# Kernel tuning notes

Hardware: AMD Instinct MI355X
Metric: run time of the kernel (lower is better)

Reference implementation:

```python
import jax, jax.numpy as jnp
import numpy as np

B, S, E, M, N, H = 16, 4096, 1024, 64, 32, 8
MIN_NODES = 3

def _ln(x, w, b, eps=1e-5):
    mu = jnp.mean(x, axis=-1, keepdims=True)
    var = jnp.mean((x - mu) ** 2, axis=-1, keepdims=True)
    return (x - mu) / jnp.sqrt(var + eps) * w + b

def setup_inputs():
    ks = jax.random.split(jax.random.key(0), 16)
    f32 = jnp.float32
    r = lambda i, shape, s: jax.random.normal(ks[i], shape, dtype=f32) * s
    return {
        "x": jax.random.normal(ks[0], (B, S, E), dtype=f32),
        "task_query": jax.random.normal(ks[1], (1, 1, E), dtype=f32),
        "wq": r(2, (E, E), 0.02), "bq": jnp.zeros((E,), f32),
        "wk": r(3, (E, E), 0.02), "bk": jnp.zeros((E,), f32),
        "wv": r(4, (E, E), 0.02), "bv": jnp.zeros((E,), f32),
        "wo": r(5, (E, E), 0.02), "bo": jnp.zeros((E,), f32),
        "mp_w": r(6, (M, E), 0.02), "mp_b": jnp.zeros((M,), f32),
        "ln_w": jnp.ones((M,), f32), "ln_b": jnp.zeros((M,), f32),
        "ng_w1": r(7, (2 * M, M), 0.05), "ng_b1": jnp.zeros((2 * M,), f32),
        "ng_w2": r(8, (N * M, 2 * M), 0.05), "ng_b2": jnp.zeros((N * M,), f32),
        "imp_w": r(9, (1, M), 0.1), "imp_b": jnp.zeros((1,), f32),
        "ep_w": r(10, (1, M, M), 0.05), "ep_b": jnp.zeros((1,), f32),
        "cp_w1": r(11, (M // 2, M), 0.1), "cp_b1": jnp.zeros((M // 2,), f32),
        "cp_w2": r(12, (1, M // 2), 0.1), "cp_b2": jnp.zeros((1,), f32),
        "np_w": r(13, (E, M), 0.05), "np_b": jnp.zeros((E,), f32),
    }

def reference(x, task_query, wq, bq, wk, bk, wv, bv, wo, bo, mp_w, mp_b,
              ln_w, ln_b, ng_w1, ng_b1, ng_w2, ng_b2, imp_w, imp_b,
              ep_w, ep_b, cp_w1, cp_b1, cp_w2, cp_b2, np_w, np_b):
    Bx, Sx, Ex = x.shape
    D = Ex // H
    # multi-head attention: single learned task query attends over x (q_len=1)
    q = jnp.broadcast_to(task_query, (Bx, 1, Ex)) @ wq.T + bq
    k = x @ wk.T + bk
    v = x @ wv.T + bv
    qh = q.reshape(Bx, 1, H, D).transpose(0, 2, 1, 3)
    kh = k.reshape(Bx, Sx, H, D).transpose(0, 2, 1, 3)
    vh = v.reshape(Bx, Sx, H, D).transpose(0, 2, 1, 3)
    attn = jax.nn.softmax(jnp.einsum('bhqd,bhkd->bhqk', qh, kh) / jnp.sqrt(jnp.float32(D)), axis=-1)
    ctx = jnp.einsum('bhqk,bhkd->bhqd', attn, vh).transpose(0, 2, 1, 3).reshape(Bx, 1, Ex)
    task_repr = (ctx @ wo.T + bo)[:, 0, :]  # (B, E)
    # manifold projection + node generation
    tm = _ln(task_repr @ mp_w.T + mp_b, ln_w, ln_b)  # (B, M)
    h = jax.nn.gelu(tm @ ng_w1.T + ng_b1, approximate=False)
    nm = (h @ ng_w2.T + ng_b2).reshape(Bx, N, M)
    nm = _ln(nm, ln_w, ln_b)  # (B, N, M)
    # deterministic node selection via top-k importance
    importance = nm @ imp_w[0] + imp_b[0]  # (B, N)
    k_nodes = max(MIN_NODES, min(N, Sx // 2 + 1))
    _, top_idx = jax.lax.top_k(importance, k_nodes)
    node_mask = jnp.zeros((Bx, N), dtype=bool).at[jnp.arange(Bx)[:, None], top_idx].set(True)
    # pairwise bilinear edge scoring as ONE batched contraction (replaces NxN python loop)
    edge_logits = jnp.einsum('bim,mn,bjn->bij', nm, ep_w[0], nm) + ep_b[0]
    dag_mask = jnp.triu(jnp.ones((N, N), x.dtype), k=1)
    pair_mask = (node_mask[:, :, None] & node_mask[:, None, :]).astype(x.dtype)
    adj = jax.nn.sigmoid(edge_logits) * dag_mask * pair_mask
    adj_matrix = (adj > 0.3).astype(x.dtype)
    # complexity / surface area
    c = jax.nn.gelu(nm @ cp_w1.T + cp_b1, approximate=False)
    c = (c @ cp_w2.T + cp_b2)[..., 0]
    complexities = jax.nn.softplus(c) * node_mask.astype(x.dtype)
    surface_area = complexities.sum(-1)
    node_embeddings = nm @ np_w.T + np_b  # (B, N, E)
    return node_embeddings, adj_matrix, surface_area, complexities, node_mask
```

## Files before the change

### kernel.cpp

```cpp
#include <hip/hip_runtime.h>
#include <hip/hip_bf16.h>


#define DEVFN __device__ __forceinline__

constexpr float SCALE = 0.08838834764831845f;

constexpr size_t OFF_QVEC  = 0;
constexpr size_t OFF_QKT   = 1024;
constexpr size_t OFF_QB    = 9216;
constexpr size_t OFF_LPART = 9224;
constexpr size_t OFF_CTX   = 13320;
constexpr size_t OFF_TREP  = 29704;
constexpr size_t OFF_TM    = 46088;
constexpr size_t OFF_NMG   = 47112;
constexpr size_t OFF_PART  = 79880;

constexpr size_t OUT_EMB  = 0;
constexpr size_t OUT_ADJ  = 524288;
constexpr size_t OUT_SURF = 540672;
constexpr size_t OUT_CPLX = 540688;
constexpr size_t OUT_MASK = 541200;

DEVFN float gelu_exact(float x) {
  return 0.5f * x * (1.0f + erff(x * 0.70710678118654752f));
}
DEVFN float softplus_f(float x) {
  return fmaxf(x, 0.0f) + log1pf(expf(-fabsf(x)));
}
DEVFN float dot4(float4 a, float4 b) {
  return a.x * b.x + a.y * b.y + a.z * b.z + a.w * b.w;
}

__global__ void k_qvec(const float* __restrict__ tq, const float* __restrict__ wq,
                       const float* __restrict__ bq, float* __restrict__ qvec) {
  int wid = threadIdx.x >> 6, lane = threadIdx.x & 63;
  int i = blockIdx.x * 4 + wid;
  const float* wrow = wq + (size_t)i * 1024;
  float acc = 0.f;
#pragma unroll
  for (int k = 0; k < 4; ++k) {
    int e = lane * 4 + k * 256;
    acc += dot4(*(const float4*)(tq + e), *(const float4*)(wrow + e));
  }
#pragma unroll
  for (int off = 32; off; off >>= 1) acc += __shfl_xor(acc, off);
  if (lane == 0) qvec[i] = acc + bq[i];
}

__global__ void k_qk(const float* __restrict__ qvec, const float* __restrict__ wk,
                     const float* __restrict__ bk, float* __restrict__ qkT,
                     float* __restrict__ qb) {
  __shared__ float qh[128];
  int h = blockIdx.x >> 2, e0 = (blockIdx.x & 3) * 256;
  int t = threadIdx.x;
  if (t < 128) qh[t] = qvec[h * 128 + t];
  __syncthreads();
  int e = e0 + t;
  float acc = 0.f;
#pragma unroll 32
  for (int d = 0; d < 128; ++d)
    acc += qh[d] * wk[(size_t)(h * 128 + d) * 1024 + e];
  qkT[h * 1024 + e] = acc * SCALE;
  if (t == 0 && e0 == 0) {
    float s = 0.f;
    for (int d = 0; d < 128; ++d) s += qh[d] * bk[h * 128 + d];
    qb[h] = s * SCALE;
  }
}

__global__ __launch_bounds__(256, 2) void k_fused(
    const float* __restrict__ x, const float* __restrict__ qkT,
    const float* __restrict__ qb, float* __restrict__ partial,
    float* __restrict__ lpart) {
  __shared__ __align__(16) float lds[8 * 1024];
  __shared__ float s_ll[8];
  int t = threadIdx.x, wid = t >> 6, lane = t & 63;
  int rh = wid >> 1, hg = wid & 1;

  float4 qr[4][4];
#pragma unroll
  for (int hh = 0; hh < 4; ++hh)
#pragma unroll
    for (int k = 0; k < 4; ++k)
      qr[hh][k] = *(const float4*)(qkT + (hg * 4 + hh) * 1024 + k * 256 + lane * 4);
  float qbr[4];
#pragma unroll
  for (int hh = 0; hh < 4; ++hh) qbr[hh] = qb[hg * 4 + hh];

  float4 acc[4][4];
#pragma unroll
  for (int hh = 0; hh < 4; ++hh)
#pragma unroll
    for (int k = 0; k < 4; ++k) acc[hh][k] = make_float4(0.f, 0.f, 0.f, 0.f);
  float lsum[4] = {0.f, 0.f, 0.f, 0.f};

  int row0 = blockIdx.x * 128 + rh * 64;
  const float* xr = x + ((size_t)row0 << 10) + lane * 4;
  float4 A0 = *(const float4*)(xr + 0);
  float4 A1 = *(const float4*)(xr + 256);
  float4 A2 = *(const float4*)(xr + 512);
  float4 A3 = *(const float4*)(xr + 768);
  float4 B0 = *(const float4*)(xr + 1024);
  float4 B1 = *(const float4*)(xr + 1280);
  float4 B2 = *(const float4*)(xr + 1536);
  float4 B3 = *(const float4*)(xr + 1792);

  for (int r = 0; r < 64; ++r) {
    float4 c0 = A0, c1 = A1, c2 = A2, c3 = A3;
    A0 = B0; A1 = B1; A2 = B2; A3 = B3;
    if (r < 62) {
      const float* nx = xr + ((size_t)(r + 2) << 10);
      B0 = *(const float4*)(nx + 0);
      B1 = *(const float4*)(nx + 256);
      B2 = *(const float4*)(nx + 512);
      B3 = *(const float4*)(nx + 768);
    }
    float s[4];
#pragma unroll
    for (int hh = 0; hh < 4; ++hh)
      s[hh] = dot4(c0, qr[hh][0]) + dot4(c1, qr[hh][1]) +
              dot4(c2, qr[hh][2]) + dot4(c3, qr[hh][3]);
#pragma unroll
    for (int off = 1; off <= 32; off <<= 1)
#pragma unroll
      for (int hh = 0; hh < 4; ++hh) s[hh] += __shfl_xor(s[hh], off);
    float w[4];
#pragma unroll
    for (int hh = 0; hh < 4; ++hh) {
      w[hh] = expf(s[hh] + qbr[hh]);
      lsum[hh] += w[hh];
    }
#pragma unroll
    for (int hh = 0; hh < 4; ++hh) {
      acc[hh][0].x += w[hh] * c0.x; acc[hh][0].y += w[hh] * c0.y;
      acc[hh][0].z += w[hh] * c0.z; acc[hh][0].w += w[hh] * c0.w;
      acc[hh][1].x += w[hh] * c1.x; acc[hh][1].y += w[hh] * c1.y;
      acc[hh][1].z += w[hh] * c1.z; acc[hh][1].w += w[hh] * c1.w;
      acc[hh][2].x += w[hh] * c2.x; acc[hh][2].y += w[hh] * c2.y;
      acc[hh][2].z += w[hh] * c2.z; acc[hh][2].w += w[hh] * c2.w;
      acc[hh][3].x += w[hh] * c3.x; acc[hh][3].y += w[hh] * c3.y;
      acc[hh][3].z += w[hh] * c3.z; acc[hh][3].w += w[hh] * c3.w;
    }
  }
  if (rh == 1) {
#pragma unroll
    for (int hh = 0; hh < 4; ++hh)
#pragma unroll
      for (int k = 0; k < 4; ++k)
        *(float4*)(lds + (hg * 4 + hh) * 1024 + k * 256 + lane * 4) = acc[hh][k];
    if (lane == 0)
#pragma unroll
      for (int hh = 0; hh < 4; ++hh) s_ll[hg * 4 + hh] = lsum[hh];
  }
  __syncthreads();
  if (rh == 0) {
    size_t base = (((size_t)blockIdx.x * 8 + hg * 4) << 10) + lane * 4;
#pragma unroll
    for (int hh = 0; hh < 4; ++hh)
#pragma unroll
      for (int k = 0; k < 4; ++k) {
        const float4 o = *(const float4*)(lds + (hg * 4 + hh) * 1024 + k * 256 + lane * 4);
        float4 v = acc[hh][k];
        v.x += o.x; v.y += o.y; v.z += o.z; v.w += o.w;
        *(float4*)(partial + base + ((size_t)hh << 10) + k * 256) = v;
      }
    if (lane == 0)
#pragma unroll
      for (int hh = 0; hh < 4; ++hh)
        lpart[blockIdx.x * 8 + hg * 4 + hh] = lsum[hh] + s_ll[hg * 4 + hh];
  }
}

__global__ __launch_bounds__(256) void k_combctx(
    const float* __restrict__ partial, const float* __restrict__ lpart,
    const float* __restrict__ wv, const float* __restrict__ bv,
    float* __restrict__ ctx) {
  __shared__ __align__(16) float s_xa[1024];
  __shared__ float s_linv;
  int bh = blockIdx.x, b = bh >> 3, h = bh & 7, t = threadIdx.x;
  float4 s4 = make_float4(0.f, 0.f, 0.f, 0.f);
#pragma unroll 8
  for (int c = 0; c < 32; ++c) {
    float4 v = *(const float4*)(partial +
        (((size_t)(b * 32 + c) * 8 + h) << 10) + t * 4);
    s4.x += v.x; s4.y += v.y; s4.z += v.z; s4.w += v.w;
  }
  *(float4*)(s_xa + t * 4) = s4;
  if (t == 0) {
    float s = 0.f;
#pragma unroll
    for (int c = 0; c < 32; ++c) s += lpart[(b * 32 + c) * 8 + h];
    s_linv = 1.0f / s;
  }
  __syncthreads();
  int wid = t >> 6, lane = t & 63;
  float linv = s_linv;
  for (int it = 0; it < 32; ++it) {
    int j = h * 128 + wid * 32 + it;
    const float* wr = wv + (size_t)j * 1024 + lane * 4;
    const float* xr = s_xa + lane * 4;
    float acc = 0.f;
#pragma unroll
    for (int k = 0; k < 4; ++k)
      acc += dot4(*(const float4*)(xr + k * 256), *(const float4*)(wr + k * 256));
#pragma unroll
    for (int off = 32; off; off >>= 1) acc += __shfl_xor(acc, off);
    if (lane == 0) ctx[b * 1024 + j] = acc * linv + bv[j];
  }
}

__global__ void k_trep(const float* __restrict__ ctx, const float* __restrict__ wo,
                       const float* __restrict__ bo, float* __restrict__ trep) {
  int wid = threadIdx.x >> 6, lane = threadIdx.x & 63;
#pragma unroll
  for (int it = 0; it < 4; ++it) {
    int gw = blockIdx.x * 16 + wid * 4 + it;
    int b = gw >> 10, i = gw & 1023;
    const float* xr = ctx + (size_t)b * 1024;
    const float* wr = wo + (size_t)i * 1024;
    float acc = 0.f;
#pragma unroll
    for (int k = 0; k < 4; ++k) {
      int e = lane * 4 + k * 256;
      acc += dot4(*(const float4*)(xr + e), *(const float4*)(wr + e));
    }
#pragma unroll
    for (int off = 32; off; off >>= 1) acc += __shfl_xor(acc, off);
    if (lane == 0) trep[b * 1024 + i] = acc + bo[i];
  }
}

__global__ void k_tm(const float* __restrict__ trep, const float* __restrict__ mp_w,
                     const float* __restrict__ mp_b, float* __restrict__ tmg) {
  int b = blockIdx.x >> 2, mc = blockIdx.x & 3;
  int wid = threadIdx.x >> 6, lane = threadIdx.x & 63;
  const float* xr = trep + (size_t)b * 1024 + lane * 4;
#pragma unroll
  for (int it = 0; it < 4; ++it) {
    int m = mc * 16 + wid * 4 + it;
    const float* wr = mp_w + (size_t)m * 1024 + lane * 4;
    float acc = 0.f;
#pragma unroll
    for (int k = 0; k < 4; ++k)
      acc += dot4(*(const float4*)(xr + k * 256), *(const float4*)(wr + k * 256));
#pragma unroll
    for (int off = 32; off; off >>= 1) acc += __shfl_xor(acc, off);
    if (lane == 0) tmg[b * 64 + m] = acc + mp_b[m];
  }
}

__global__ __launch_bounds__(256) void k_nm(
    const float* __restrict__ tmg, const float* __restrict__ ln_w,
    const float* __restrict__ ln_b, const float* __restrict__ ng_w1,
    const float* __restrict__ ng_b1, const float* __restrict__ ng_w2,
    const float* __restrict__ ng_b2, float* __restrict__ nmg) {
  __shared__ float s_tm[64];
  __shared__ float s_h2[128];
  __shared__ float s_np[128];
  int b = blockIdx.x >> 4, np = blockIdx.x & 15;
  int t = threadIdx.x, wid = t >> 6, lane = t & 63;
  if (wid == 0) {
    float v = tmg[b * 64 + lane];
    float sm = v;
#pragma unroll
    for (int off = 32; off; off >>= 1) sm += __shfl_xor(sm, off);
    float mu = sm * (1.f / 64.f);
    float d = v - mu;
    float vv = d * d;
#pragma unroll
    for (int off = 32; off; off >>= 1) vv += __shfl_xor(vv, off);
    float rstd = 1.f / sqrtf(vv * (1.f / 64.f) + 1e-5f);
    s_tm[lane] = d * rstd * ln_w[lane] + ln_b[lane];
  }
  __syncthreads();
  if (t < 128) {
    float acc = ng_b1[t];
    const float* wr = ng_w1 + (size_t)t * 64;
#pragma unroll 16
    for (int m = 0; m < 64; ++m) acc += s_tm[m] * wr[m];
    s_h2[t] = gelu_exact(acc);
  }
  __syncthreads();
  if (t < 128) {
    int o = np * 128 + t;
    float acc = ng_b2[o];
    const float* wr = ng_w2 + (size_t)o * 128;
#pragma unroll 8
    for (int r = 0; r < 128; ++r) acc += s_h2[r] * wr[r];
    s_np[t] = acc;
  }
  __syncthreads();
  if (wid < 2) {
    float v = s_np[wid * 64 + lane];
    float sm = v;
#pragma unroll
    for (int off = 32; off; off >>= 1) sm += __shfl_xor(sm, off);
    float mu = sm * (1.f / 64.f);
    float d = v - mu;
    float vv = d * d;
#pragma unroll
    for (int off = 32; off; off >>= 1) vv += __shfl_xor(vv, off);
    float rstd = 1.f / sqrtf(vv * (1.f / 64.f) + 1e-5f);
    nmg[b * 2048 + (np * 2 + wid) * 64 + lane] = d * rstd * ln_w[lane] + ln_b[lane];
  }
}

__global__ __launch_bounds__(256) void k_headsemb(
    const float* __restrict__ nmg, const float* __restrict__ ep_w,
    const float* __restrict__ ep_b, const float* __restrict__ cp_w1,
    const float* __restrict__ cp_b1, const float* __restrict__ cp_w2,
    const float* __restrict__ cp_b2, const float* __restrict__ np_w,
    const float* __restrict__ np_b, float* __restrict__ out) {
  __shared__ __align__(16) float s_nm[2048];
  __shared__ float s_t[2048];
  __shared__ float s_c1[1024];
  __shared__ float s_cx[32];
  int t = threadIdx.x, wid = t >> 6, lane = t & 63;
  if (blockIdx.x < 16) {
    int b = blockIdx.x;
    for (int i = t; i < 512; i += 256)
      ((float4*)s_nm)[i] = ((const float4*)(nmg + (size_t)b * 2048))[i];
    __syncthreads();
    for (int o = t; o < 1024; o += 256) {
      int i = o >> 5, r = o & 31;
      float acc = cp_b1[r];
      const float* wr = cp_w1 + (size_t)r * 64;
#pragma unroll 8
      for (int m = 0; m < 64; ++m) acc += s_nm[i * 64 + m] * wr[m];
      s_c1[o] = gelu_exact(acc);
    }
    __syncthreads();
    if (t < 32) {
      float acc = cp_b2[0];
#pragma unroll 8
      for (int r = 0; r < 32; ++r) acc += s_c1[t * 32 + r] * cp_w2[r];
      float sp = softplus_f(acc);
      s_cx[t] = sp;
      out[OUT_CPLX + b * 32 + t] = sp;
      out[OUT_MASK + b * 32 + t] = 1.0f;
    }
    __syncthreads();
    if (wid == 0) {
      float v = (lane < 32) ? s_cx[lane] : 0.f;
#pragma unroll
      for (int off = 32; off; off >>= 1) v += __shfl_xor(v, off);
      if (lane == 0) out[OUT_SURF + b] = v;
    }
    for (int o = t; o < 2048; o += 256) {
      int i = o >> 6, n = o & 63;
      float acc = 0.f;
#pragma unroll 8
      for (int m = 0; m < 64; ++m) acc += s_nm[i * 64 + m] * ep_w[m * 64 + n];
      s_t[o] = acc;
    }
    __syncthreads();
    for (int o = t; o < 1024; o += 256) {
      int i = o >> 5, j = o & 31;
      float acc = ep_b[0];
#pragma unroll 8
      for (int n = 0; n < 64; ++n) acc += s_t[i * 64 + n] * s_nm[j * 64 + n];
      float sg = 1.f / (1.f + expf(-acc));
      float val = (j > i && sg > 0.3f) ? 1.f : 0.f;
      out[OUT_ADJ + (size_t)b * 1024 + i * 32 + j] = val;
    }
  } else {
    int idx = blockIdx.x - 16;
    int b = idx >> 2, e0 = (idx & 3) * 256;
    *(float4*)(s_nm + t * 4) = *(const float4*)(nmg + b * 2048 + t * 4);
    *(float4*)(s_nm + 1024 + t * 4) =
        *(const float4*)(nmg + b * 2048 + 1024 + t * 4);
    __syncthreads();
    int e = e0 + t;
    float4 w[16];
    const float* wr = np_w + (size_t)e * 64;
#pragma unroll
    for (int k = 0; k < 16; ++k) w[k] = *(const float4*)(wr + k * 4);
    float bias = np_b[e];
    for (int i = 0; i < 32; ++i) {
      float acc = bias;
#pragma unroll
      for (int k = 0; k < 16; ++k)
        acc += dot4(w[k], *(const float4*)(s_nm + i * 64 + k * 4));
      out[OUT_EMB + (size_t)(b * 32 + i) * 1024 + e] = acc;
    }
  }
}

extern "C" void kernel_launch(void* const* d_in, const int* in_sizes, int n_in,
                              void* d_out, int out_size, void* d_ws, size_t ws_size,
                              hipStream_t stream) {
  (void)in_sizes; (void)n_in; (void)out_size; (void)ws_size;
  const float* x    = (const float*)d_in[0];
  const float* tq   = (const float*)d_in[1];
  const float* wq   = (const float*)d_in[2];
  const float* bq   = (const float*)d_in[3];
  const float* wk   = (const float*)d_in[4];
  const float* bk   = (const float*)d_in[5];
  const float* wv   = (const float*)d_in[6];
  const float* bv   = (const float*)d_in[7];
  const float* wo   = (const float*)d_in[8];
  const float* bo   = (const float*)d_in[9];
  const float* mp_w = (const float*)d_in[10];
  const float* mp_b = (const float*)d_in[11];
  const float* ln_w = (const float*)d_in[12];
  const float* ln_b = (const float*)d_in[13];
  const float* ng_w1 = (const float*)d_in[14];
  const float* ng_b1 = (const float*)d_in[15];
  const float* ng_w2 = (const float*)d_in[16];
  const float* ng_b2 = (const float*)d_in[17];
  const float* ep_w  = (const float*)d_in[20];
  const float* ep_b  = (const float*)d_in[21];
  const float* cp_w1 = (const float*)d_in[22];
  const float* cp_b1 = (const float*)d_in[23];
  const float* cp_w2 = (const float*)d_in[24];
  const float* cp_b2 = (const float*)d_in[25];
  const float* np_w  = (const float*)d_in[26];
  const float* np_b  = (const float*)d_in[27];

  float* out = (float*)d_out;
  float* ws = (float*)d_ws;
  float* qvec    = ws + OFF_QVEC;
  float* qkT     = ws + OFF_QKT;
  float* qb      = ws + OFF_QB;
  float* lpart   = ws + OFF_LPART;
  float* ctx     = ws + OFF_CTX;
  float* trep    = ws + OFF_TREP;
  float* tmg     = ws + OFF_TM;
  float* nmg     = ws + OFF_NMG;
  float* partial = ws + OFF_PART;

  k_qvec<<<256, 256, 0, stream>>>(tq, wq, bq, qvec);
  k_qk<<<32, 256, 0, stream>>>(qvec, wk, bk, qkT, qb);
  k_fused<<<512, 256, 0, stream>>>(x, qkT, qb, partial, lpart);
  k_combctx<<<128, 256, 0, stream>>>(partial, lpart, wv, bv, ctx);
  k_trep<<<1024, 256, 0, stream>>>(ctx, wo, bo, trep);
  k_tm<<<64, 256, 0, stream>>>(trep, mp_w, mp_b, tmg);
  k_nm<<<256, 256, 0, stream>>>(tmg, ln_w, ln_b, ng_w1, ng_b1, ng_w2, ng_b2, nmg);
  k_headsemb<<<80, 256, 0, stream>>>(nmg, ep_w, ep_b, cp_w1, cp_b1, cp_w2,
                                     cp_b2, np_w, np_b, out);
}
```

Before: 178.3 us.

## Fuse tail kernels into one persistent kernel with software grid barriers

Merges the five post-attention kernels (ctx combine, output projection, mp projection, node generation, heads/embeddings) into a single 128-block kernel that separates stages with an atomic-counter grid barrier. The aim is to remove four kernel launch gaps on a tail made of small, latency-bound GEMVs. The wo projection now runs on 128 blocks instead of 1024, and the ng_w2 GEMV is restructured with half-wave float4 dot products. The risks are reduced parallelism for the wo GEMV, barrier spin overhead, and reliance on all 128 blocks being co-resident. An extra memset is added to reset the barrier counters.

```diff
diff --git a/kernel.cpp b/kernel.cpp
--- a/kernel.cpp
+++ b/kernel.cpp
@@ -15,6 +15,7 @@
 constexpr size_t OFF_TM    = 46088;
 constexpr size_t OFF_NMG   = 47112;
 constexpr size_t OFF_PART  = 79880;
+constexpr size_t OFF_BAR   = 4274184;
 
 constexpr size_t OUT_EMB  = 0;
 constexpr size_t OUT_ADJ  = 524288;
@@ -22,6 +23,8 @@
 constexpr size_t OUT_CPLX = 540688;
 constexpr size_t OUT_MASK = 541200;
 
+constexpr int TAIL_BLOCKS = 128;
+
 DEVFN float gelu_exact(float x) {
   return 0.5f * x * (1.0f + erff(x * 0.70710678118654752f));
 }
@@ -30,6 +33,29 @@
 }
 DEVFN float dot4(float4 a, float4 b) {
   return a.x * b.x + a.y * b.y + a.z * b.z + a.w * b.w;
+}
+
+DEVFN void grid_sync(int* counter, unsigned int* gen) {
+  __threadfence();
+  __syncthreads();
+  if (threadIdx.x == 0) {
+    unsigned int g = __hip_atomic_load(gen, __ATOMIC_ACQUIRE,
+                                       __HIP_MEMORY_SCOPE_AGENT);
+    int arrived = __hip_atomic_fetch_add(counter, 1, __ATOMIC_ACQ_REL,
+                                         __HIP_MEMORY_SCOPE_AGENT) + 1;
+    if (arrived == TAIL_BLOCKS) {
+      __hip_atomic_store(counter, 0, __ATOMIC_RELAXED,
+                         __HIP_MEMORY_SCOPE_AGENT);
+      __hip_atomic_fetch_add(gen, 1u, __ATOMIC_ACQ_REL,
+                             __HIP_MEMORY_SCOPE_AGENT);
+    } else {
+      while (__hip_atomic_load(gen, __ATOMIC_ACQUIRE,
+                               __HIP_MEMORY_SCOPE_AGENT) == g)
+        __builtin_amdgcn_s_sleep(2);
+    }
+  }
+  __syncthreads();
+  __threadfence();
 }
 
 __global__ void k_qvec(const float* __restrict__ tq, const float* __restrict__ wq,
@@ -140,7 +166,7 @@
       acc[hh][2].x += w[hh] * c2.x; acc[hh][2].y += w[hh] * c2.y;
       acc[hh][2].z += w[hh] * c2.z; acc[hh][2].w += w[hh] * c2.w;
       acc[hh][3].x += w[hh] * c3.x; acc[hh][3].y += w[hh] * c3.y;
-      acc[hh][3].z += w[hh] * c3.z; acc[hh][3].w += w[hh] * c3.w;
+      acc[hh][3].w += w[hh] * c3.w; acc[hh][3].z += w[hh] * c3.z;
     }
   }
   if (rh == 1) {
@@ -172,153 +198,161 @@
   }
 }
 
-__global__ __launch_bounds__(256) void k_combctx(
+__global__ __launch_bounds__(256) void k_tailp(
     const float* __restrict__ partial, const float* __restrict__ lpart,
     const float* __restrict__ wv, const float* __restrict__ bv,
-    float* __restrict__ ctx) {
-  __shared__ __align__(16) float s_xa[1024];
-  __shared__ float s_linv;
-  int bh = blockIdx.x, b = bh >> 3, h = bh & 7, t = threadIdx.x;
-  float4 s4 = make_float4(0.f, 0.f, 0.f, 0.f);
+    const float* __restrict__ wo, const float* __restrict__ bo,
+    const float* __restrict__ mp_w, const float* __restrict__ mp_b,
+    const float* __restrict__ ln_w, const float* __restrict__ ln_b,
+    const float* __restrict__ ng_w1, const float* __restrict__ ng_b1,
+    const float* __restrict__ ng_w2, const float* __restrict__ ng_b2,
+    const float* __restrict__ ep_w, const float* __restrict__ ep_b,
+    const float* __restrict__ cp_w1, const float* __restrict__ cp_b1,
+    const float* __restrict__ cp_w2, const float* __restrict__ cp_b2,
+    const float* __restrict__ np_w, const float* __restrict__ np_b,
+    float* __restrict__ ctx, float* __restrict__ trep,
+    float* __restrict__ tmg, float* __restrict__ nmg,
+    int* __restrict__ bar_counter, unsigned int* __restrict__ bar_gen,
+    float* __restrict__ out) {
+  __shared__ __align__(16) float smem[5184];
+  __shared__ float s_misc;
+  int blk = blockIdx.x, t = threadIdx.x, wid = t >> 6, lane = t & 63;
+
+  {
+    int b = blk >> 3, h = blk & 7;
+    float4 s4 = make_float4(0.f, 0.f, 0.f, 0.f);
 #pragma unroll 8
-  for (int c = 0; c < 32; ++c) {
-    float4 v = *(const float4*)(partial +
-        (((size_t)(b * 32 + c) * 8 + h) << 10) + t * 4);
-    s4.x += v.x; s4.y += v.y; s4.z += v.z; s4.w += v.w;
-  }
-  *(float4*)(s_xa + t * 4) = s4;
-  if (t == 0) {
-    float s = 0.f;
-#pragma unroll
-    for (int c = 0; c < 32; ++c) s += lpart[(b * 32 + c) * 8 + h];
-    s_linv = 1.0f / s;
-  }
-  __syncthreads();
-  int wid = t >> 6, lane = t & 63;
-  float linv = s_linv;
-  for (int it = 0; it < 32; ++it) {
-    int j = h * 128 + wid * 32 + it;
-    const float* wr = wv + (size_t)j * 1024 + lane * 4;
-    const float* xr = s_xa + lane * 4;
-    float acc = 0.f;
-#pragma unroll
-    for (int k = 0; k < 4; ++k)
-      acc += dot4(*(const float4*)(xr + k * 256), *(const float4*)(wr + k * 256));
-#pragma unroll
-    for (int off = 32; off; off >>= 1) acc += __shfl_xor(acc, off);
-    if (lane == 0) ctx[b * 1024 + j] = acc * linv + bv[j];
-  }
-}
-
-__global__ void k_trep(const float* __restrict__ ctx, const float* __restrict__ wo,
-                       const float* __restrict__ bo, float* __restrict__ trep) {
-  int wid = threadIdx.x >> 6, lane = threadIdx.x & 63;
-#pragma unroll
-  for (int it = 0; it < 4; ++it) {
-    int gw = blockIdx.x * 16 + wid * 4 + it;
-    int b = gw >> 10, i = gw & 1023;
-    const float* xr = ctx + (size_t)b * 1024;
-    const float* wr = wo + (size_t)i * 1024;
-    float acc = 0.f;
-#pragma unroll
-    for (int k = 0; k < 4; ++k) {
-      int e = lane * 4 + k * 256;
-      acc += dot4(*(const float4*)(xr + e), *(const float4*)(wr + e));
-    }
-#pragma unroll
-    for (int off = 32; off; off >>= 1) acc += __shfl_xor(acc, off);
-    if (lane == 0) trep[b * 1024 + i] = acc + bo[i];
-  }
-}
-
-__global__ void k_tm(const float* __restrict__ trep, const float* __restrict__ mp_w,
-                     const float* __restrict__ mp_b, float* __restrict__ tmg) {
-  int b = blockIdx.x >> 2, mc = blockIdx.x & 3;
-  int wid = threadIdx.x >> 6, lane = threadIdx.x & 63;
-  const float* xr = trep + (size_t)b * 1024 + lane * 4;
-#pragma unroll
-  for (int it = 0; it < 4; ++it) {
-    int m = mc * 16 + wid * 4 + it;
-    const float* wr = mp_w + (size_t)m * 1024 + lane * 4;
-    float acc = 0.f;
-#pragma unroll
-    for (int k = 0; k < 4; ++k)
-      acc += dot4(*(const float4*)(xr + k * 256), *(const float4*)(wr + k * 256));
-#pragma unroll
-    for (int off = 32; off; off >>= 1) acc += __shfl_xor(acc, off);
-    if (lane == 0) tmg[b * 64 + m] = acc + mp_b[m];
-  }
-}
-
-__global__ __launch_bounds__(256) void k_nm(
-    const float* __restrict__ tmg, const float* __restrict__ ln_w,
-    const float* __restrict__ ln_b, const float* __restrict__ ng_w1,
-    const float* __restrict__ ng_b1, const float* __restrict__ ng_w2,
-    const float* __restrict__ ng_b2, float* __restrict__ nmg) {
-  __shared__ float s_tm[64];
-  __shared__ float s_h2[128];
-  __shared__ float s_np[128];
-  int b = blockIdx.x >> 4, np = blockIdx.x & 15;
-  int t = threadIdx.x, wid = t >> 6, lane = t & 63;
-  if (wid == 0) {
-    float v = tmg[b * 64 + lane];
-    float sm = v;
-#pragma unroll
-    for (int off = 32; off; off >>= 1) sm += __shfl_xor(sm, off);
-    float mu = sm * (1.f / 64.f);
-    float d = v - mu;
-    float vv = d * d;
-#pragma unroll
-    for (int off = 32; off; off >>= 1) vv += __shfl_xor(vv, off);
-    float rstd = 1.f / sqrtf(vv * (1.f / 64.f) + 1e-5f);
-    s_tm[lane] = d * rstd * ln_w[lane] + ln_b[lane];
-  }
-  __syncthreads();
-  if (t < 128) {
-    float acc = ng_b1[t];
-    const float* wr = ng_w1 + (size_t)t * 64;
+    for (int c = 0; c < 32; ++c) {
+      float4 v = *(const float4*)(partial +
+          (((size_t)(b * 32 + c) * 8 + h) << 10) + t * 4);
+      s4.x += v.x; s4.y += v.y; s4.z += v.z; s4.w += v.w;
+    }
+    *(float4*)(smem + t * 4) = s4;
+    if (t == 0) {
+      float s = 0.f;
+#pragma unroll
+      for (int c = 0; c < 32; ++c) s += lpart[(b * 32 + c) * 8 + h];
+      s_misc = 1.0f / s;
+    }
+    __syncthreads();
+    float linv = s_misc;
+    for (int it = 0; it < 32; ++it) {
+      int j = h * 128 + wid * 32 + it;
+      const float* wr = wv + (size_t)j * 1024 + lane * 4;
+      const float* xr = smem + lane * 4;
+      float acc = 0.f;
+#pragma unroll
+      for (int k = 0; k < 4; ++k)
+        acc += dot4(*(const float4*)(xr + k * 256), *(const float4*)(wr + k * 256));
+#pragma unroll
+      for (int off = 32; off; off >>= 1) acc += __shfl_xor(acc, off);
+      if (lane == 0) ctx[b * 1024 + j] = acc * linv + bv[j];
+    }
+  }
+  grid_sync(bar_counter, bar_gen);
+
+  {
+    int b = blk >> 3, ch = blk & 7;
+    *(float4*)(smem + t * 4) = *(const float4*)(ctx + b * 1024 + t * 4);
+    __syncthreads();
+    for (int it = 0; it < 32; ++it) {
+      int i = ch * 128 + wid * 32 + it;
+      const float* wr = wo + (size_t)i * 1024 + lane * 4;
+      const float* xr = smem + lane * 4;
+      float acc = 0.f;
+#pragma unroll
+      for (int k = 0; k < 4; ++k)
+        acc += dot4(*(const float4*)(xr + k * 256), *(const float4*)(wr + k * 256));
+#pragma unroll
+      for (int off = 32; off; off >>= 1) acc += __shfl_xor(acc, off);
+      if (lane == 0) trep[b * 1024 + i] = acc + bo[i];
+    }
+  }
+  grid_sync(bar_counter, bar_gen);
+
+  {
+    int b = blk >> 3, mg = blk & 7;
+    *(float4*)(smem + t * 4) = *(const float4*)(trep + b * 1024 + t * 4);
+    __syncthreads();
+#pragma unroll
+    for (int it = 0; it < 2; ++it) {
+      int m = mg * 8 + wid * 2 + it;
+      const float* wr = mp_w + (size_t)m * 1024 + lane * 4;
+      const float* xr = smem + lane * 4;
+      float acc = 0.f;
+#pragma unroll
+      for (int k = 0; k < 4; ++k)
+        acc += dot4(*(const float4*)(xr + k * 256), *(const float4*)(wr + k * 256));
+#pragma unroll
+      for (int off = 32; off; off >>= 1) acc += __shfl_xor(acc, off);
+      if (lane == 0) tmg[b * 64 + m] = acc + mp_b[m];
+    }
+  }
+  grid_sync(bar_counter, bar_gen);
+
+  {
+    int b = blk >> 3, ng = blk & 7;
+    float* s_tm = smem;
+    float* s_h2 = smem + 128;
+    float* s_np = smem + 256;
+    if (wid == 0) {
+      float v = tmg[b * 64 + lane];
+      float sm = v;
+#pragma unroll
+      for (int off = 32; off; off >>= 1) sm += __shfl_xor(sm, off);
+      float mu = sm * (1.f / 64.f);
+      float d = v - mu;
+      float vv = d * d;
+#pragma unroll
+      for (int off = 32; off; off >>= 1) vv += __shfl_xor(vv, off);
+      float rstd = 1.f / sqrtf(vv * (1.f / 64.f) + 1e-5f);
+      s_tm[lane] = d * rstd * ln_w[lane] + ln_b[lane];
+    }
+    __syncthreads();
+    if (t < 128) {
+      float acc = ng_b1[t];
+      const float* wr = ng_w1 + (size_t)t * 64;
 #pragma unroll 16
-    for (int m = 0; m < 64; ++m) acc += s_tm[m] * wr[m];
-    s_h2[t] = gelu_exact(acc);
-  }
-  __syncthreads();
-  if (t < 128) {
-    int o = np * 128 + t;
-    float acc = ng_b2[o];
-    const float* wr = ng_w2 + (size_t)o * 128;
-#pragma unroll 8
-    for (int r = 0; r < 128; ++r) acc += s_h2[r] * wr[r];
-    s_np[t] = acc;
-  }
-  __syncthreads();
-  if (wid < 2) {
-    float v = s_np[wid * 64 + lane];
-    float sm = v;
-#pragma unroll
-    for (int off = 32; off; off >>= 1) sm += __shfl_xor(sm, off);
-    float mu = sm * (1.f / 64.f);
-    float d = v - mu;
-    float vv = d * d;
-#pragma unroll
-    for (int off = 32; off; off >>= 1) vv += __shfl_xor(vv, off);
-    float rstd = 1.f / sqrtf(vv * (1.f / 64.f) + 1e-5f);
-    nmg[b * 2048 + (np * 2 + wid) * 64 + lane] = d * rstd * ln_w[lane] + ln_b[lane];
-  }
-}
-
-__global__ __launch_bounds__(256) void k_headsemb(
-    const float* __restrict__ nmg, const float* __restrict__ ep_w,
-    const float* __restrict__ ep_b, const float* __restrict__ cp_w1,
-    const float* __restrict__ cp_b1, const float* __restrict__ cp_w2,
-    const float* __restrict__ cp_b2, const float* __restrict__ np_w,
-    const float* __restrict__ np_b, float* __restrict__ out) {
-  __shared__ __align__(16) float s_nm[2048];
-  __shared__ float s_t[2048];
-  __shared__ float s_c1[1024];
-  __shared__ float s_cx[32];
-  int t = threadIdx.x, wid = t >> 6, lane = t & 63;
-  if (blockIdx.x < 16) {
-    int b = blockIdx.x;
+      for (int m = 0; m < 64; ++m) acc += s_tm[m] * wr[m];
+      s_h2[t] = gelu_exact(acc);
+    }
+    __syncthreads();
+    int half = lane >> 5, hl = lane & 31;
+    float4 hv4 = *(const float4*)(s_h2 + hl * 4);
+    for (int it = 0; it < 32; ++it) {
+      int ol = wid * 64 + it * 2 + half;
+      int o = ng * 256 + ol;
+      float4 wv4 = *(const float4*)(ng_w2 + (size_t)o * 128 + hl * 4);
+      float a = dot4(wv4, hv4);
+#pragma unroll
+      for (int off = 1; off <= 16; off <<= 1) a += __shfl_xor(a, off);
+      if (hl == 0) s_np[ol] = a + ng_b2[o];
+    }
+    __syncthreads();
+    {
+      float v = s_np[wid * 64 + lane];
+      float sm = v;
+#pragma unroll
+      for (int off = 32; off; off >>= 1) sm += __shfl_xor(sm, off);
+      float mu = sm * (1.f / 64.f);
+      float d = v - mu;
+      float vv = d * d;
+#pragma unroll
+      for (int off = 32; off; off >>= 1) vv += __shfl_xor(vv, off);
+      float rstd = 1.f / sqrtf(vv * (1.f / 64.f) + 1e-5f);
+      nmg[b * 2048 + (ng * 4 + wid) * 64 + lane] =
+          d * rstd * ln_w[lane] + ln_b[lane];
+    }
+  }
+  grid_sync(bar_counter, bar_gen);
+
+  if (blk >= 80) return;
+  float* s_nm = smem;
+  float* s_t  = smem + 2048;
+  float* s_c1 = smem + 4096;
+  float* s_cx = smem + 5120;
+  if (blk < 16) {
+    int b = blk;
     for (int i = t; i < 512; i += 256)
       ((float4*)s_nm)[i] = ((const float4*)(nmg + (size_t)b * 2048))[i];
     __syncthreads();
@@ -365,7 +399,7 @@
       out[OUT_ADJ + (size_t)b * 1024 + i * 32 + j] = val;
     }
   } else {
-    int idx = blockIdx.x - 16;
+    int idx = blk - 16;
     int b = idx >> 2, e0 = (idx & 3) * 256;
     *(float4*)(s_nm + t * 4) = *(const float4*)(nmg + b * 2048 + t * 4);
     *(float4*)(s_nm + 1024 + t * 4) =
@@ -429,14 +463,15 @@
   float* tmg     = ws + OFF_TM;
   float* nmg     = ws + OFF_NMG;
   float* partial = ws + OFF_PART;
-
+  int* bar_counter = (int*)(ws + OFF_BAR);
+  unsigned int* bar_gen = (unsigned int*)(ws + OFF_BAR + 1);
+
+  hipMemsetAsync(ws + OFF_BAR, 0, 16, stream);
   k_qvec<<<256, 256, 0, stream>>>(tq, wq, bq, qvec);
   k_qk<<<32, 256, 0, stream>>>(qvec, wk, bk, qkT, qb);
   k_fused<<<512, 256, 0, stream>>>(x, qkT, qb, partial, lpart);
-  k_combctx<<<128, 256, 0, stream>>>(partial, lpart, wv, bv, ctx);
-  k_trep<<<1024, 256, 0, stream>>>(ctx, wo, bo, trep);
-  k_tm<<<64, 256, 0, stream>>>(trep, mp_w, mp_b, tmg);
-  k_nm<<<256, 256, 0, stream>>>(tmg, ln_w, ln_b, ng_w1, ng_b1, ng_w2, ng_b2, nmg);
-  k_headsemb<<<80, 256, 0, stream>>>(nmg, ep_w, ep_b, cp_w1, cp_b1, cp_w2,
-                                     cp_b2, np_w, np_b, out);
-}
+  k_tailp<<<TAIL_BLOCKS, 256, 0, stream>>>(
+      partial, lpart, wv, bv, wo, bo, mp_w, mp_b, ln_w, ln_b, ng_w1, ng_b1,
+      ng_w2, ng_b2, ep_w, ep_b, cp_w1, cp_b1, cp_w2, cp_b2, np_w, np_b,
+      ctx, trep, tmg, nmg, bar_counter, bar_gen, out);
+}
```

New measurement: 308.7 us. +73.2%, slower.

## Precompose V, output and task projections into one weight, drop ctx/trep kernels

Applied to the files above, without the earlier changes.

Folds the chain wv -> wo -> mp_w into one precomputed 64x8x1024 matrix (W3 = mp_w·wo·wv per head) plus folded bias vectors. The attention-weighted x sums then go straight to the 64-dim task vector in a single kernel, replacing the combctx, trep and tm kernels. This removes the per-batch 1024x1024 GEMVs over wv and wo, but every call now has to compute the weight products in prep kernels, whose strided column reads of wo and wv are costly. The ng_w2 stage is also reworked to use coalesced float4 row loads with half-wave reductions and fewer blocks.

```diff
diff --git a/kernel.cpp b/kernel.cpp
--- a/kernel.cpp
+++ b/kernel.cpp
@@ -10,11 +10,13 @@
 constexpr size_t OFF_QKT   = 1024;
 constexpr size_t OFF_QB    = 9216;
 constexpr size_t OFF_LPART = 9224;
-constexpr size_t OFF_CTX   = 13320;
-constexpr size_t OFF_TREP  = 29704;
-constexpr size_t OFF_TM    = 46088;
-constexpr size_t OFF_NMG   = 47112;
-constexpr size_t OFF_PART  = 79880;
+constexpr size_t OFF_W2T   = 13320;
+constexpr size_t OFF_W3    = 78856;
+constexpr size_t OFF_B2A   = 603144;
+constexpr size_t OFF_B2B   = 603208;
+constexpr size_t OFF_TM    = 603272;
+constexpr size_t OFF_NMG   = 604296;
+constexpr size_t OFF_PART  = 637064;
 
 constexpr size_t OUT_EMB  = 0;
 constexpr size_t OUT_ADJ  = 524288;
@@ -32,40 +34,147 @@
   return a.x * b.x + a.y * b.y + a.z * b.z + a.w * b.w;
 }
 
-__global__ void k_qvec(const float* __restrict__ tq, const float* __restrict__ wq,
-                       const float* __restrict__ bq, float* __restrict__ qvec) {
-  int wid = threadIdx.x >> 6, lane = threadIdx.x & 63;
-  int i = blockIdx.x * 4 + wid;
-  const float* wrow = wq + (size_t)i * 1024;
-  float acc = 0.f;
-#pragma unroll
-  for (int k = 0; k < 4; ++k) {
-    int e = lane * 4 + k * 256;
-    acc += dot4(*(const float4*)(tq + e), *(const float4*)(wrow + e));
-  }
-#pragma unroll
-  for (int off = 32; off; off >>= 1) acc += __shfl_xor(acc, off);
-  if (lane == 0) qvec[i] = acc + bq[i];
-}
-
-__global__ void k_qk(const float* __restrict__ qvec, const float* __restrict__ wk,
-                     const float* __restrict__ bk, float* __restrict__ qkT,
-                     float* __restrict__ qb) {
-  __shared__ float qh[128];
-  int h = blockIdx.x >> 2, e0 = (blockIdx.x & 3) * 256;
-  int t = threadIdx.x;
-  if (t < 128) qh[t] = qvec[h * 128 + t];
+__global__ __launch_bounds__(256) void k_pre1(
+    const float* __restrict__ tq, const float* __restrict__ wq,
+    const float* __restrict__ bq, const float* __restrict__ wo,
+    const float* __restrict__ mp_w, float* __restrict__ qvec,
+    float* __restrict__ w2t) {
+  __shared__ float s_w2[4][64][17];
+  int t = threadIdx.x, wid = t >> 6, lane = t & 63;
+  if (blockIdx.x < 256) {
+    int i = blockIdx.x * 4 + wid;
+    const float* wrow = wq + (size_t)i * 1024;
+    float acc = 0.f;
+#pragma unroll
+    for (int k = 0; k < 4; ++k) {
+      int e = lane * 4 + k * 256;
+      acc += dot4(*(const float4*)(tq + e), *(const float4*)(wrow + e));
+    }
+#pragma unroll
+    for (int off = 32; off; off >>= 1) acc += __shfl_xor(acc, off);
+    if (lane == 0) qvec[i] = acc + bq[i];
+    return;
+  }
+  int idx = blockIdx.x - 256;
+  int jb = idx & 15, mc = idx >> 4;
+  int j = jb * 64 + lane;
+  float acc[16];
+#pragma unroll
+  for (int mm = 0; mm < 16; ++mm) acc[mm] = 0.f;
+  const float* wop = wo + (size_t)(wid * 256) * 1024 + j;
+  const float* mpp = mp_w + (size_t)(mc * 16) * 1024 + wid * 256;
+  for (int i = 0; i < 256; ++i) {
+    float wov = wop[(size_t)i * 1024];
+#pragma unroll
+    for (int mm = 0; mm < 16; ++mm)
+      acc[mm] += mpp[(size_t)mm * 1024 + i] * wov;
+  }
+#pragma unroll
+  for (int mm = 0; mm < 16; ++mm) s_w2[wid][lane][mm] = acc[mm];
   __syncthreads();
-  int e = e0 + t;
-  float acc = 0.f;
+  int jj = t >> 2, mq = (t & 3) * 4;
+  float4 s = make_float4(0.f, 0.f, 0.f, 0.f);
+#pragma unroll
+  for (int w = 0; w < 4; ++w) {
+    s.x += s_w2[w][jj][mq + 0];
+    s.y += s_w2[w][jj][mq + 1];
+    s.z += s_w2[w][jj][mq + 2];
+    s.w += s_w2[w][jj][mq + 3];
+  }
+  *(float4*)(w2t + (size_t)(jb * 64 + jj) * 64 + mc * 16 + mq) = s;
+}
+
+__global__ __launch_bounds__(256) void k_pre2(
+    const float* __restrict__ qvec, const float* __restrict__ wk,
+    const float* __restrict__ bk, const float* __restrict__ wv,
+    const float* __restrict__ bv, const float* __restrict__ bo,
+    const float* __restrict__ mp_w, const float* __restrict__ mp_b,
+    const float* __restrict__ w2t, float* __restrict__ qkT,
+    float* __restrict__ qb, float* __restrict__ w3,
+    float* __restrict__ b2a, float* __restrict__ b2b) {
+  __shared__ float smem[256];
+  int blk = blockIdx.x, t = threadIdx.x, wid = t >> 6, lane = t & 63;
+  if (blk < 32) {
+    __shared__ float qh[128];
+    int h = blk >> 2, e0 = (blk & 3) * 256;
+    if (t < 128) qh[t] = qvec[h * 128 + t];
+    __syncthreads();
+    int e = e0 + t;
+    float acc = 0.f;
 #pragma unroll 32
-  for (int d = 0; d < 128; ++d)
-    acc += qh[d] * wk[(size_t)(h * 128 + d) * 1024 + e];
-  qkT[h * 1024 + e] = acc * SCALE;
-  if (t == 0 && e0 == 0) {
-    float s = 0.f;
-    for (int d = 0; d < 128; ++d) s += qh[d] * bk[h * 128 + d];
-    qb[h] = s * SCALE;
+    for (int d = 0; d < 128; ++d)
+      acc += qh[d] * wk[(size_t)(h * 128 + d) * 1024 + e];
+    qkT[h * 1024 + e] = acc * SCALE;
+    if (t == 0 && e0 == 0) {
+      float s = 0.f;
+      for (int d = 0; d < 128; ++d) s += qh[d] * bk[h * 128 + d];
+      qb[h] = s * SCALE;
+    }
+    return;
+  }
+  if (blk < 96) {
+    int idx = blk - 32;
+    int h = idx >> 3, ec = (idx >> 1) & 3, mh = idx & 1;
+    int e = ec * 256 + t;
+    float acc[32];
+#pragma unroll
+    for (int m = 0; m < 32; ++m) acc[m] = 0.f;
+    const float* wvp = wv + (size_t)(h * 128) * 1024 + e;
+    const float* w2p = w2t + (size_t)(h * 128) * 64 + mh * 32;
+    for (int jjj = 0; jjj < 128; ++jjj) {
+      float wvv = wvp[(size_t)jjj * 1024];
+      const float* w2row = w2p + (size_t)jjj * 64;
+#pragma unroll
+      for (int m = 0; m < 32; ++m) acc[m] += w2row[m] * wvv;
+    }
+#pragma unroll
+    for (int m = 0; m < 32; ++m)
+      w3[((size_t)(mh * 32 + m) * 8 + h) * 1024 + e] = acc[m];
+    return;
+  }
+  if (blk == 96) {
+    float acc[64];
+#pragma unroll
+    for (int m = 0; m < 64; ++m) acc[m] = 0.f;
+#pragma unroll
+    for (int jq = 0; jq < 4; ++jq) {
+      int j = t * 4 + jq;
+      float bvj = bv[j];
+      const float* row = w2t + (size_t)j * 64;
+#pragma unroll
+      for (int k = 0; k < 16; ++k) {
+        float4 r = *(const float4*)(row + k * 4);
+        acc[k * 4 + 0] += bvj * r.x;
+        acc[k * 4 + 1] += bvj * r.y;
+        acc[k * 4 + 2] += bvj * r.z;
+        acc[k * 4 + 3] += bvj * r.w;
+      }
+    }
+#pragma unroll
+    for (int m = 0; m < 64; ++m) {
+#pragma unroll
+      for (int off = 32; off; off >>= 1) acc[m] += __shfl_xor(acc[m], off);
+    }
+    if (lane == 0) {
+#pragma unroll
+      for (int m = 0; m < 64; ++m) smem[wid * 64 + m] = acc[m];
+    }
+    __syncthreads();
+    if (t < 64)
+      b2a[t] = smem[t] + smem[64 + t] + smem[128 + t] + smem[192 + t];
+    return;
+  }
+  for (int it = 0; it < 16; ++it) {
+    int m = wid * 16 + it;
+    const float* wr = mp_w + (size_t)m * 1024 + lane * 4;
+    const float* br = bo + lane * 4;
+    float a = 0.f;
+#pragma unroll
+    for (int k = 0; k < 4; ++k)
+      a += dot4(*(const float4*)(wr + k * 256), *(const float4*)(br + k * 256));
+#pragma unroll
+    for (int off = 32; off; off >>= 1) a += __shfl_xor(a, off);
+    if (lane == 0) b2b[m] = a + mp_b[m];
   }
 }
 
@@ -172,81 +281,51 @@
   }
 }
 
-__global__ __launch_bounds__(256) void k_combctx(
+__global__ __launch_bounds__(256) void k_tmb(
     const float* __restrict__ partial, const float* __restrict__ lpart,
-    const float* __restrict__ wv, const float* __restrict__ bv,
-    float* __restrict__ ctx) {
-  __shared__ __align__(16) float s_xa[1024];
-  __shared__ float s_linv;
-  int bh = blockIdx.x, b = bh >> 3, h = bh & 7, t = threadIdx.x;
-  float4 s4 = make_float4(0.f, 0.f, 0.f, 0.f);
+    const float* __restrict__ w3, const float* __restrict__ b2a,
+    const float* __restrict__ b2b, float* __restrict__ tmg) {
+  __shared__ __align__(16) float s_xa[8192];
+  __shared__ float s_red[32];
+  __shared__ float s_linv[8];
+  int blk = blockIdx.x, b = blk >> 2, mc = blk & 3;
+  int t = threadIdx.x, wid = t >> 6, lane = t & 63;
+  {
+    int h = lane & 7, c = wid * 8 + (lane >> 3);
+    float v = lpart[(size_t)(b * 32 + c) * 8 + h];
+    v += __shfl_xor(v, 8);
+    v += __shfl_xor(v, 16);
+    v += __shfl_xor(v, 32);
+    if (lane < 8) s_red[wid * 8 + lane] = v;
+    __syncthreads();
+    if (t < 8)
+      s_linv[t] = 1.0f / (s_red[t] + s_red[8 + t] + s_red[16 + t] + s_red[24 + t]);
+    __syncthreads();
+  }
+  for (int h = 0; h < 8; ++h) {
+    float4 a = make_float4(0.f, 0.f, 0.f, 0.f);
+    const float* pp = partial + (size_t)b * 262144 + h * 1024 + t * 4;
 #pragma unroll 8
-  for (int c = 0; c < 32; ++c) {
-    float4 v = *(const float4*)(partial +
-        (((size_t)(b * 32 + c) * 8 + h) << 10) + t * 4);
-    s4.x += v.x; s4.y += v.y; s4.z += v.z; s4.w += v.w;
-  }
-  *(float4*)(s_xa + t * 4) = s4;
-  if (t == 0) {
-    float s = 0.f;
-#pragma unroll
-    for (int c = 0; c < 32; ++c) s += lpart[(b * 32 + c) * 8 + h];
-    s_linv = 1.0f / s;
+    for (int c = 0; c < 32; ++c) {
+      float4 v = *(const float4*)(pp + (size_t)c * 8192);
+      a.x += v.x; a.y += v.y; a.z += v.z; a.w += v.w;
+    }
+    float li = s_linv[h];
+    a.x *= li; a.y *= li; a.z *= li; a.w *= li;
+    *(float4*)(s_xa + h * 1024 + t * 4) = a;
   }
   __syncthreads();
-  int wid = t >> 6, lane = t & 63;
-  float linv = s_linv;
-  for (int it = 0; it < 32; ++it) {
-    int j = h * 128 + wid * 32 + it;
-    const float* wr = wv + (size_t)j * 1024 + lane * 4;
+  for (int q = 0; q < 4; ++q) {
+    int m = mc * 16 + wid * 4 + q;
+    const float* w3r = w3 + (size_t)m * 8192 + lane * 4;
     const float* xr = s_xa + lane * 4;
-    float acc = 0.f;
-#pragma unroll
-    for (int k = 0; k < 4; ++k)
-      acc += dot4(*(const float4*)(xr + k * 256), *(const float4*)(wr + k * 256));
-#pragma unroll
-    for (int off = 32; off; off >>= 1) acc += __shfl_xor(acc, off);
-    if (lane == 0) ctx[b * 1024 + j] = acc * linv + bv[j];
-  }
-}
-
-__global__ void k_trep(const float* __restrict__ ctx, const float* __restrict__ wo,
-                       const float* __restrict__ bo, float* __restrict__ trep) {
-  int wid = threadIdx.x >> 6, lane = threadIdx.x & 63;
-#pragma unroll
-  for (int it = 0; it < 4; ++it) {
-    int gw = blockIdx.x * 16 + wid * 4 + it;
-    int b = gw >> 10, i = gw & 1023;
-    const float* xr = ctx + (size_t)b * 1024;
-    const float* wr = wo + (size_t)i * 1024;
-    float acc = 0.f;
-#pragma unroll
-    for (int k = 0; k < 4; ++k) {
-      int e = lane * 4 + k * 256;
-      acc += dot4(*(const float4*)(xr + e), *(const float4*)(wr + e));
-    }
-#pragma unroll
-    for (int off = 32; off; off >>= 1) acc += __shfl_xor(acc, off);
-    if (lane == 0) trep[b * 1024 + i] = acc + bo[i];
-  }
-}
-
-__global__ void k_tm(const float* __restrict__ trep, const float* __restrict__ mp_w,
-                     const float* __restrict__ mp_b, float* __restrict__ tmg) {
-  int b = blockIdx.x >> 2, mc = blockIdx.x & 3;
-  int wid = threadIdx.x >> 6, lane = threadIdx.x & 63;
-  const float* xr = trep + (size_t)b * 1024 + lane * 4;
-#pragma unroll
-  for (int it = 0; it < 4; ++it) {
-    int m = mc * 16 + wid * 4 + it;
-    const float* wr = mp_w + (size_t)m * 1024 + lane * 4;
-    float acc = 0.f;
-#pragma unroll
-    for (int k = 0; k < 4; ++k)
-      acc += dot4(*(const float4*)(xr + k * 256), *(const float4*)(wr + k * 256));
-#pragma unroll
-    for (int off = 32; off; off >>= 1) acc += __shfl_xor(acc, off);
-    if (lane == 0) tmg[b * 64 + m] = acc + mp_b[m];
+    float a = 0.f;
+#pragma unroll
+    for (int k = 0; k < 32; ++k)
+      a += dot4(*(const float4*)(w3r + k * 256), *(const float4*)(xr + k * 256));
+#pragma unroll
+    for (int off = 32; off; off >>= 1) a += __shfl_xor(a, off);
+    if (lane == 0) tmg[b * 64 + m] = a + b2a[m] + b2b[m];
   }
 }
 
@@ -257,8 +336,8 @@
     const float* __restrict__ ng_b2, float* __restrict__ nmg) {
   __shared__ float s_tm[64];
   __shared__ float s_h2[128];
-  __shared__ float s_np[128];
-  int b = blockIdx.x >> 4, np = blockIdx.x & 15;
+  __shared__ float s_np[256];
+  int b = blockIdx.x >> 3, ng = blockIdx.x & 7;
   int t = threadIdx.x, wid = t >> 6, lane = t & 63;
   if (wid == 0) {
     float v = tmg[b * 64 + lane];
@@ -282,16 +361,19 @@
     s_h2[t] = gelu_exact(acc);
   }
   __syncthreads();
-  if (t < 128) {
-    int o = np * 128 + t;
-    float acc = ng_b2[o];
-    const float* wr = ng_w2 + (size_t)o * 128;
-#pragma unroll 8
-    for (int r = 0; r < 128; ++r) acc += s_h2[r] * wr[r];
-    s_np[t] = acc;
+  int half = lane >> 5, hl = lane & 31;
+  float4 hv4 = *(const float4*)(s_h2 + hl * 4);
+  for (int it = 0; it < 32; ++it) {
+    int ol = wid * 64 + it * 2 + half;
+    int o = ng * 256 + ol;
+    float4 wv4 = *(const float4*)(ng_w2 + (size_t)o * 128 + hl * 4);
+    float a = dot4(wv4, hv4);
+#pragma unroll
+    for (int off = 1; off <= 16; off <<= 1) a += __shfl_xor(a, off);
+    if (hl == 0) s_np[ol] = a + ng_b2[o];
   }
   __syncthreads();
-  if (wid < 2) {
+  {
     float v = s_np[wid * 64 + lane];
     float sm = v;
 #pragma unroll
@@ -302,11 +384,12 @@
 #pragma unroll
     for (int off = 32; off; off >>= 1) vv += __shfl_xor(vv, off);
     float rstd = 1.f / sqrtf(vv * (1.f / 64.f) + 1e-5f);
-    nmg[b * 2048 + (np * 2 + wid) * 64 + lane] = d * rstd * ln_w[lane] + ln_b[lane];
-  }
-}
-
-__global__ __launch_bounds__(256) void k_headsemb(
+    nmg[b * 2048 + (ng * 4 + wid) * 64 + lane] =
+        d * rstd * ln_w[lane] + ln_b[lane];
+  }
+}
+
+__global__ __launch_bounds__(256) void k_he(
     const float* __restrict__ nmg, const float* __restrict__ ep_w,
     const float* __restrict__ ep_b, const float* __restrict__ cp_w1,
     const float* __restrict__ cp_b1, const float* __restrict__ cp_w2,
@@ -424,19 +507,20 @@
   float* qkT     = ws + OFF_QKT;
   float* qb      = ws + OFF_QB;
   float* lpart   = ws + OFF_LPART;
-  float* ctx     = ws + OFF_CTX;
-  float* trep    = ws + OFF_TREP;
+  float* w2t     = ws + OFF_W2T;
+  float* w3      = ws + OFF_W3;
+  float* b2a     = ws + OFF_B2A;
+  float* b2b     = ws + OFF_B2B;
   float* tmg     = ws + OFF_TM;
   float* nmg     = ws + OFF_NMG;
   float* partial = ws + OFF_PART;
 
-  k_qvec<<<256, 256, 0, stream>>>(tq, wq, bq, qvec);
-  k_qk<<<32, 256, 0, stream>>>(qvec, wk, bk, qkT, qb);
+  k_pre1<<<320, 256, 0, stream>>>(tq, wq, bq, wo, mp_w, qvec, w2t);
+  k_pre2<<<98, 256, 0, stream>>>(qvec, wk, bk, wv, bv, bo, mp_w, mp_b, w2t,
+                                 qkT, qb, w3, b2a, b2b);
   k_fused<<<512, 256, 0, stream>>>(x, qkT, qb, partial, lpart);
-  k_combctx<<<128, 256, 0, stream>>>(partial, lpart, wv, bv, ctx);
-  k_trep<<<1024, 256, 0, stream>>>(ctx, wo, bo, trep);
-  k_tm<<<64, 256, 0, stream>>>(trep, mp_w, mp_b, tmg);
-  k_nm<<<256, 256, 0, stream>>>(tmg, ln_w, ln_b, ng_w1, ng_b1, ng_w2, ng_b2, nmg);
-  k_headsemb<<<80, 256, 0, stream>>>(nmg, ep_w, ep_b, cp_w1, cp_b1, cp_w2,
-                                     cp_b2, np_w, np_b, out);
-}
+  k_tmb<<<64, 256, 0, stream>>>(partial, lpart, w3, b2a, b2b, tmg);
+  k_nm<<<128, 256, 0, stream>>>(tmg, ln_w, ln_b, ng_w1, ng_b1, ng_w2, ng_b2, nmg);
+  k_he<<<80, 256, 0, stream>>>(nmg, ep_w, ep_b, cp_w1, cp_b1, cp_w2, cp_b2,
+                               np_w, np_b, out);
+}
```

Result: slower. 300.9 us (+68.8%).
